# Performance work log

Hardware: AMD Instinct MI355X
Metric: run time of the kernel (lower is better)

## Reference

```python
import jax, jax.numpy as jnp
import numpy as np

TAU = 0.5
EPS = 1e-08


def setup_inputs() -> dict:
    key = jax.random.key(0)
    k1, k2 = jax.random.split(key)
    B, D = 8192, 128
    z_a = jax.random.normal(k1, (B, D), dtype=jnp.float32)
    z_b = jax.random.normal(k2, (B, D), dtype=jnp.float32)
    return {"z_a": z_a, "z_b": z_b}


def reference(z_a, z_b):
    B = z_a.shape[0]
    N = 2 * B
    z = jnp.concatenate([z_a, z_b], axis=0)           # [2B, D]
    sim = (z @ z.T) / TAU                             # [2B, 2B]
    sp = jax.nn.softplus(sim)
    # zero out self-similarity (diagonal)
    idx = jnp.arange(N)
    sp = sp.at[idx, idx].set(0.0)
    denom = jnp.maximum(sp.sum(axis=-1), EPS)         # [2B]
    pos_idx = (idx + B) % N
    sp_pos = sp[idx, pos_idx]                         # [2B]
    log_p = jnp.log(jnp.maximum(sp_pos, EPS)) - jnp.log(denom)
    return -log_p.mean()
```

## Files before the change

kernel.cpp:

```cpp
#include <hip/hip_runtime.h>
#include <hip/hip_bf16.h>

constexpr int Bh = 8192;
constexpr int Nn = 16384;
constexpr int Dd = 128;
constexpr float EPS = 1e-8f;
constexpr float LN2 = 0.69314718056f;

constexpr int K_TILES = 16;
constexpr int N_TILES = 16512;
constexpr int N_BLOCKS = N_TILES / K_TILES;

typedef short bf16x8 __attribute__((ext_vector_type(8)));
typedef float f32x4 __attribute__((ext_vector_type(4)));

__global__ __launch_bounds__(256) void convert_kernel(const float4* __restrict__ za,
                                                      const float4* __restrict__ zb,
                                                      ushort* __restrict__ z,
                                                      float* __restrict__ rowsum,
                                                      float* __restrict__ out) {
    const int t = blockIdx.x * 256 + threadIdx.x;
    constexpr int Q = (Bh * Dd) / 4;
    const float SCL = 1.69864363f;
    float4 v = (t < Q) ? za[t] : zb[t - Q];
    union { ushort4 u4; __hip_bfloat16 h[4]; } cv;
    cv.h[0] = __float2bfloat16(v.x * SCL);
    cv.h[1] = __float2bfloat16(v.y * SCL);
    cv.h[2] = __float2bfloat16(v.z * SCL);
    cv.h[3] = __float2bfloat16(v.w * SCL);
    ((ushort4*)z)[t] = cv.u4;
    if (t < Nn) rowsum[t] = 0.f;
    if (t == 0) out[0] = 0.f;
}

__device__ __forceinline__ int row_tile_of(int g) {
    int t = (int)((257.0f - sqrtf((float)(66049 - 4 * g))) * 0.5f);
    t = t < 0 ? 0 : (t > 127 ? 127 : t);
    while (t * (257 - t) > g) --t;
    while ((t + 1) * (256 - t) <= g) ++t;
    return t;
}

__device__ __forceinline__ void flush_rs(float* __restrict__ rowsum, int rowW,
                                         float (&rs)[2][4], int q, int c) {
#pragma unroll
    for (int s = 0; s < 2; ++s)
#pragma unroll
        for (int r = 0; r < 4; ++r) {
            float v = rs[s][r];
            v += __shfl_xor(v, 1);
            v += __shfl_xor(v, 2);
            v += __shfl_xor(v, 4);
            v += __shfl_xor(v, 8);
            if (c == 0) atomicAdd(&rowsum[rowW + s * 16 + q * 4 + r], v);
            rs[s][r] = 0.f;
        }
}

__device__ __forceinline__ void colflush(float* __restrict__ rowsum,
                                         float (&csumP)[4], int C0P, int lane, int c) {
#pragma unroll
    for (int st = 0; st < 4; ++st) {
        float v = csumP[st];
        v += __shfl_xor(v, 16);
        v += __shfl_xor(v, 32);
        if (lane < 16) atomicAdd(&rowsum[C0P + st * 16 + c], v);
    }
}

__device__ __forceinline__ void stage_tile(const ushort* __restrict__ z, ushort* lbuf,
                                           int C0, int wave, int lane) {
#pragma unroll
    for (int i = 0; i < 4; ++i) {
        const int chunk = wave * 4 + i;
        const int r = (chunk << 2) + (lane >> 4);
        const int bl = ((lane & 15) ^ (r & 15)) << 4;
        const char* gp = (const char*)z + (((size_t)(C0 + r)) << 8) + bl;
        ushort* lp = lbuf + (chunk << 9);
        __builtin_amdgcn_global_load_lds((const __attribute__((address_space(1))) void*)gp,
                                         (__attribute__((address_space(3))) void*)lp,
                                         16, 0, 0);
    }
}

__global__ __launch_bounds__(256) void main_kernel(const ushort* __restrict__ z,
                                                   float* __restrict__ rowsum,
                                                   float* __restrict__ pospair) {
    __shared__ ushort ldsb[2][8192];

    const int tid = threadIdx.x;
    const int wave = tid >> 6;
    const int lane = tid & 63;
    const int q = lane >> 4;
    const int c = lane & 15;
    const int g0 = blockIdx.x * K_TILES;

    int tr = row_tile_of(g0);
    int ct = 2 * tr + (g0 - tr * (257 - tr));

    int O[4];
#pragma unroll
    for (int kt = 0; kt < 4; ++kt) O[kt] = (c << 8) + ((((q + 4 * kt) ^ c)) << 4);

    bf16x8 afrag[2][4];
    float rs[2][4];
#pragma unroll
    for (int s = 0; s < 2; ++s)
#pragma unroll
        for (int r = 0; r < 4; ++r) rs[s][r] = 0.f;

    const f32x4 Z4 = {0.f, 0.f, 0.f, 0.f};

    float csumP[4];
    int C0P = 0;
    bool pendP = false;
    int cur_tr = -1, rowW = 0, cur = 0;

    stage_tile(z, &ldsb[0][0], ct << 6, wave, lane);
    __syncthreads();

    for (int j = 0; j < K_TILES; ++j) {
        const int C0 = ct << 6;
        const bool diag = ((ct >> 1) == tr);

        if (tr != cur_tr) {
            if (cur_tr >= 0) flush_rs(rowsum, rowW, rs, q, c);
            cur_tr = tr;
            rowW = (tr << 7) + wave * 32;
#pragma unroll
            for (int s = 0; s < 2; ++s) {
                const ushort* ap = z + (size_t)(rowW + s * 16 + c) * Dd;
#pragma unroll
                for (int kt = 0; kt < 4; ++kt)
                    afrag[s][kt] = *(const bf16x8*)(ap + kt * 32 + q * 8);
            }
        }

        if (pendP) { colflush(rowsum, csumP, C0P, lane, c); pendP = false; }

        int trN = tr, ctN = ct + 1;
        if (ctN == 256) { trN = tr + 1; ctN = 2 * trN; }
        if (j + 1 < K_TILES) stage_tile(z, &ldsb[cur ^ 1][0], ctN << 6, wave, lane);

        const char* lb = (const char*)&ldsb[cur][0];
        float csum[4];
#pragma unroll
        for (int st = 0; st < 4; ++st) csum[st] = 0.f;

        f32x4 acc[2][2];
#pragma unroll
        for (int st = 0; st < 5; ++st) {
            const int p = st & 1;
            if (st < 4) {
                bf16x8 bcur[4];
#pragma unroll
                for (int kt = 0; kt < 4; ++kt)
                    bcur[kt] = *(const bf16x8*)(lb + O[kt] + st * 4096);
#pragma unroll
                for (int s = 0; s < 2; ++s)
                    acc[p][s] = __builtin_amdgcn_mfma_f32_16x16x32_bf16(afrag[s][0], bcur[0], Z4, 0, 0, 0);
#pragma unroll
                for (int kt = 1; kt < 4; ++kt) {
#pragma unroll
                    for (int s = 0; s < 2; ++s)
                        acc[p][s] = __builtin_amdgcn_mfma_f32_16x16x32_bf16(afrag[s][kt], bcur[kt], acc[p][s], 0, 0, 0);
                }
            }
            if (st > 0) {
                const int stP = st - 1;
                const int pp = p ^ 1;
                const int gc0 = C0 + stP * 16;
#pragma unroll
                for (int s = 0; s < 2; ++s) {
                    const int R = rowW + s * 16;
                    float sp[4];
#pragma unroll
                    for (int r = 0; r < 4; ++r) {
                        float u = acc[pp][s][r];
                        float e = __builtin_amdgcn_exp2f(-fabsf(u));
                        sp[r] = fmaxf(u, 0.f) + __builtin_amdgcn_logf(1.f + e);
                    }
                    if (diag && gc0 == R) {
#pragma unroll
                        for (int r = 0; r < 4; ++r)
                            if (c == q * 4 + r) sp[r] = 0.f;
                    }
                    if (gc0 == (R ^ Bh)) {
#pragma unroll
                        for (int r = 0; r < 4; ++r)
                            if (c == q * 4 + r) pospair[R + q * 4 + r] = sp[r];
                    }
#pragma unroll
                    for (int r = 0; r < 4; ++r) rs[s][r] += sp[r];
                    if (!diag) csum[stP] += (sp[0] + sp[1]) + (sp[2] + sp[3]);
                }
            }
        }

        if (!diag) {
#pragma unroll
            for (int st = 0; st < 4; ++st) csumP[st] = csum[st];
            C0P = C0;
            pendP = true;
        }

        __syncthreads();
        cur ^= 1;
        tr = trN;
        ct = ctN;
    }

    if (pendP) colflush(rowsum, csumP, C0P, lane, c);
    if (cur_tr >= 0) flush_rs(rowsum, rowW, rs, q, c);
}

__global__ __launch_bounds__(1024) void finalize_kernel(const float* __restrict__ rowsum,
                                                        const float* __restrict__ pospair,
                                                        float* __restrict__ out) {
    __shared__ float red[16];
    const int i = blockIdx.x * 1024 + threadIdx.x;
    float denom = fmaxf(LN2 * rowsum[i], EPS);
    float sp = fmaxf(LN2 * pospair[i & (Bh - 1)], EPS);
    float acc = __logf(sp) - __logf(denom);
#pragma unroll
    for (int m = 1; m < 64; m <<= 1) acc += __shfl_xor(acc, m);
    if ((threadIdx.x & 63) == 0) red[threadIdx.x >> 6] = acc;
    __syncthreads();
    if (threadIdx.x < 16) {
        float v = red[threadIdx.x];
        v += __shfl_xor(v, 1);
        v += __shfl_xor(v, 2);
        v += __shfl_xor(v, 4);
        v += __shfl_xor(v, 8);
        if (threadIdx.x == 0) atomicAdd(out, -v / (float)Nn);
    }
}

extern "C" void kernel_launch(void* const* d_in, const int* in_sizes, int n_in,
                              void* d_out, int out_size, void* d_ws, size_t ws_size,
                              hipStream_t stream) {
    const float* za = (const float*)d_in[0];
    const float* zb = (const float*)d_in[1];

    ushort* z = (ushort*)d_ws;
    float* rowsum = (float*)((char*)d_ws + (size_t)Nn * Dd * 2);
    float* pospair = rowsum + Nn;
    float* out = (float*)d_out;

    convert_kernel<<<2048, 256, 0, stream>>>((const float4*)za, (const float4*)zb, z, rowsum, out);
    main_kernel<<<N_BLOCKS, 256, 0, stream>>>(z, rowsum, pospair);
    finalize_kernel<<<16, 1024, 0, stream>>>(rowsum, pospair, out);
}
```

Measured before the change: 165.2 us.

## Fuse bf16 conversion into main kernel and finalize via last-block ticket

Removes the separate convert kernel: the main kernel now loads fp32 rows from z_a/z_b into registers, scales and converts them to bf16, and writes the result to LDS after compute, replacing async global-to-LDS loads. The finalize kernel is folded into the main kernel with an atomic ticket counter, so the last block computes the loss. The goal is fewer launches and no bf16 round trip through global memory. In exchange, global reads double in size, staging is register-based with extra conversion ALU work, and the final reduction runs serially in one block.

```diff
diff --git a/kernel.cpp b/kernel.cpp
--- a/kernel.cpp
+++ b/kernel.cpp
@@ -6,6 +6,7 @@
 constexpr int Dd = 128;
 constexpr float EPS = 1e-8f;
 constexpr float LN2 = 0.69314718056f;
+constexpr float SCL = 1.69864363f;
 
 constexpr int K_TILES = 16;
 constexpr int N_TILES = 16512;
@@ -13,25 +14,6 @@
 
 typedef short bf16x8 __attribute__((ext_vector_type(8)));
 typedef float f32x4 __attribute__((ext_vector_type(4)));
-
-__global__ __launch_bounds__(256) void convert_kernel(const float4* __restrict__ za,
-                                                      const float4* __restrict__ zb,
-                                                      ushort* __restrict__ z,
-                                                      float* __restrict__ rowsum,
-                                                      float* __restrict__ out) {
-    const int t = blockIdx.x * 256 + threadIdx.x;
-    constexpr int Q = (Bh * Dd) / 4;
-    const float SCL = 1.69864363f;
-    float4 v = (t < Q) ? za[t] : zb[t - Q];
-    union { ushort4 u4; __hip_bfloat16 h[4]; } cv;
-    cv.h[0] = __float2bfloat16(v.x * SCL);
-    cv.h[1] = __float2bfloat16(v.y * SCL);
-    cv.h[2] = __float2bfloat16(v.z * SCL);
-    cv.h[3] = __float2bfloat16(v.w * SCL);
-    ((ushort4*)z)[t] = cv.u4;
-    if (t < Nn) rowsum[t] = 0.f;
-    if (t == 0) out[0] = 0.f;
-}
 
 __device__ __forceinline__ int row_tile_of(int g) {
     int t = (int)((257.0f - sqrtf((float)(66049 - 4 * g))) * 0.5f);
@@ -68,25 +50,50 @@
     }
 }
 
-__device__ __forceinline__ void stage_tile(const ushort* __restrict__ z, ushort* lbuf,
-                                           int C0, int wave, int lane) {
+__device__ __forceinline__ void stage_load(const float* __restrict__ za,
+                                           const float* __restrict__ zb,
+                                           int C0, int wave, int lane,
+                                           float4 (&SL)[4][2]) {
 #pragma unroll
     for (int i = 0; i < 4; ++i) {
         const int chunk = wave * 4 + i;
         const int r = (chunk << 2) + (lane >> 4);
         const int bl = ((lane & 15) ^ (r & 15)) << 4;
-        const char* gp = (const char*)z + (((size_t)(C0 + r)) << 8) + bl;
-        ushort* lp = lbuf + (chunk << 9);
-        __builtin_amdgcn_global_load_lds((const __attribute__((address_space(1))) void*)gp,
-                                         (__attribute__((address_space(3))) void*)lp,
-                                         16, 0, 0);
-    }
-}
-
-__global__ __launch_bounds__(256) void main_kernel(const ushort* __restrict__ z,
+        const int r4 = C0 + r;
+        const float* base = (r4 < Bh ? za : zb) + (size_t)(r4 & (Bh - 1)) * Dd + (bl >> 1);
+        SL[i][0] = *(const float4*)(base);
+        SL[i][1] = *(const float4*)(base + 4);
+    }
+}
+
+__device__ __forceinline__ void stage_write(ushort* lbuf, int wave, int lane,
+                                            const float4 (&SL)[4][2]) {
+#pragma unroll
+    for (int i = 0; i < 4; ++i) {
+        const int chunk = wave * 4 + i;
+        union { ushort u[8]; bf16x8 v; } P;
+#pragma unroll
+        for (int h = 0; h < 2; ++h) {
+            union { float4 v; float f[4]; } X; X.v = SL[i][h];
+#pragma unroll
+            for (int k = 0; k < 4; ++k) {
+                union { __hip_bfloat16 b; ushort s; } cv;
+                cv.b = __float2bfloat16(X.f[k] * SCL);
+                P.u[h * 4 + k] = cv.s;
+            }
+        }
+        *(bf16x8*)(lbuf + (chunk << 9) + (lane << 3)) = P.v;
+    }
+}
+
+__global__ __launch_bounds__(256) void main_kernel(const float* __restrict__ za,
+                                                   const float* __restrict__ zb,
                                                    float* __restrict__ rowsum,
-                                                   float* __restrict__ pospair) {
+                                                   float* __restrict__ pospair,
+                                                   int* __restrict__ counter,
+                                                   float* __restrict__ out) {
     __shared__ ushort ldsb[2][8192];
+    __shared__ int sh_ticket;
 
     const int tid = threadIdx.x;
     const int wave = tid >> 6;
@@ -116,7 +123,9 @@
     bool pendP = false;
     int cur_tr = -1, rowW = 0, cur = 0;
 
-    stage_tile(z, &ldsb[0][0], ct << 6, wave, lane);
+    float4 SL[4][2];
+    stage_load(za, zb, ct << 6, wave, lane, SL);
+    stage_write(&ldsb[0][0], wave, lane, SL);
     __syncthreads();
 
     for (int j = 0; j < K_TILES; ++j) {
@@ -129,10 +138,23 @@
             rowW = (tr << 7) + wave * 32;
 #pragma unroll
             for (int s = 0; s < 2; ++s) {
-                const ushort* ap = z + (size_t)(rowW + s * 16 + c) * Dd;
-#pragma unroll
-                for (int kt = 0; kt < 4; ++kt)
-                    afrag[s][kt] = *(const bf16x8*)(ap + kt * 32 + q * 8);
+                const int row = rowW + s * 16 + c;
+                const float* ap = (row < Bh ? za : zb) + (size_t)(row & (Bh - 1)) * Dd;
+#pragma unroll
+                for (int kt = 0; kt < 4; ++kt) {
+                    union { float4 v; float f[4]; } X0, X1;
+                    X0.v = *(const float4*)(ap + kt * 32 + q * 8);
+                    X1.v = *(const float4*)(ap + kt * 32 + q * 8 + 4);
+                    union { ushort u[8]; bf16x8 v; } P;
+#pragma unroll
+                    for (int k = 0; k < 4; ++k) {
+                        union { __hip_bfloat16 b; ushort s; } c0, c1;
+                        c0.b = __float2bfloat16(X0.f[k] * SCL);
+                        c1.b = __float2bfloat16(X1.f[k] * SCL);
+                        P.u[k] = c0.s; P.u[4 + k] = c1.s;
+                    }
+                    afrag[s][kt] = P.v;
+                }
             }
         }
 
@@ -140,7 +162,7 @@
 
         int trN = tr, ctN = ct + 1;
         if (ctN == 256) { trN = tr + 1; ctN = 2 * trN; }
-        if (j + 1 < K_TILES) stage_tile(z, &ldsb[cur ^ 1][0], ctN << 6, wave, lane);
+        if (j + 1 < K_TILES) stage_load(za, zb, ctN << 6, wave, lane, SL);
 
         const char* lb = (const char*)&ldsb[cur][0];
         float csum[4];
@@ -188,7 +210,9 @@
                     if (gc0 == (R ^ Bh)) {
 #pragma unroll
                         for (int r = 0; r < 4; ++r)
-                            if (c == q * 4 + r) pospair[R + q * 4 + r] = sp[r];
+                            if (c == q * 4 + r)
+                                __hip_atomic_store(&pospair[R + q * 4 + r], sp[r],
+                                                   __ATOMIC_RELAXED, __HIP_MEMORY_SCOPE_AGENT);
                     }
 #pragma unroll
                     for (int r = 0; r < 4; ++r) rs[s][r] += sp[r];
@@ -203,6 +227,8 @@
             C0P = C0;
             pendP = true;
         }
+
+        if (j + 1 < K_TILES) stage_write(&ldsb[cur ^ 1][0], wave, lane, SL);
 
         __syncthreads();
         cur ^= 1;
@@ -212,27 +238,29 @@
 
     if (pendP) colflush(rowsum, csumP, C0P, lane, c);
     if (cur_tr >= 0) flush_rs(rowsum, rowW, rs, q, c);
-}
-
-__global__ __launch_bounds__(1024) void finalize_kernel(const float* __restrict__ rowsum,
-                                                        const float* __restrict__ pospair,
-                                                        float* __restrict__ out) {
-    __shared__ float red[16];
-    const int i = blockIdx.x * 1024 + threadIdx.x;
-    float denom = fmaxf(LN2 * rowsum[i], EPS);
-    float sp = fmaxf(LN2 * pospair[i & (Bh - 1)], EPS);
-    float acc = __logf(sp) - __logf(denom);
-#pragma unroll
-    for (int m = 1; m < 64; m <<= 1) acc += __shfl_xor(acc, m);
-    if ((threadIdx.x & 63) == 0) red[threadIdx.x >> 6] = acc;
+
+    __threadfence();
     __syncthreads();
-    if (threadIdx.x < 16) {
-        float v = red[threadIdx.x];
-        v += __shfl_xor(v, 1);
-        v += __shfl_xor(v, 2);
-        v += __shfl_xor(v, 4);
-        v += __shfl_xor(v, 8);
-        if (threadIdx.x == 0) atomicAdd(out, -v / (float)Nn);
+    if (tid == 0) sh_ticket = atomicAdd(counter, 1);
+    __syncthreads();
+    if (sh_ticket == N_BLOCKS - 1) {
+        __threadfence();
+        float acc = 0.f;
+        for (int i = tid; i < Nn; i += 256) {
+            float rsv = __hip_atomic_load(&rowsum[i], __ATOMIC_RELAXED, __HIP_MEMORY_SCOPE_AGENT);
+            float ppv = __hip_atomic_load(&pospair[i & (Bh - 1)], __ATOMIC_RELAXED, __HIP_MEMORY_SCOPE_AGENT);
+            float denom = fmaxf(LN2 * rsv, EPS);
+            float sp = fmaxf(LN2 * ppv, EPS);
+            acc += __logf(sp) - __logf(denom);
+        }
+#pragma unroll
+        for (int m = 1; m < 64; m <<= 1) acc += __shfl_xor(acc, m);
+        float* red = (float*)&ldsb[0][0];
+        __syncthreads();
+        if (lane == 0) red[wave] = acc;
+        __syncthreads();
+        if (tid == 0)
+            out[0] = -(red[0] + red[1] + red[2] + red[3]) / (float)Nn;
     }
 }
 
@@ -242,12 +270,11 @@
     const float* za = (const float*)d_in[0];
     const float* zb = (const float*)d_in[1];
 
-    ushort* z = (ushort*)d_ws;
-    float* rowsum = (float*)((char*)d_ws + (size_t)Nn * Dd * 2);
-    float* pospair = rowsum + Nn;
+    float* rowsum = (float*)d_ws;
+    int* counter = (int*)(rowsum + Nn);
+    float* pospair = rowsum + Nn + 64;
     float* out = (float*)d_out;
 
-    convert_kernel<<<2048, 256, 0, stream>>>((const float4*)za, (const float4*)zb, z, rowsum, out);
-    main_kernel<<<N_BLOCKS, 256, 0, stream>>>(z, rowsum, pospair);
-    finalize_kernel<<<16, 1024, 0, stream>>>(rowsum, pospair, out);
-}
+    hipMemsetAsync(rowsum, 0, (size_t)(Nn + 64) * sizeof(float), stream);
+    main_kernel<<<N_BLOCKS, 256, 0, stream>>>(za, zb, rowsum, pospair, counter, out);
+}
```

After: 289.3 us. 75.1% more time.
